# Kernel tuning notes

Measured on AMD Instinct MI355X. Metric: run time of the kernel, lower is better.

## Reference

```python
import jax, jax.numpy as jnp
import numpy as np

N_NODES = 100000
N_EDGES = 800000
N_ETYPES = 5
IN_DIM = 23
HID_DIM = 128
OUT_DIM = 64
NUM_GRAPHS = 64


def setup_inputs() -> dict:
    key = jax.random.key(0)
    ks = jax.random.split(key, 8)
    feat = jax.random.normal(ks[0], (N_NODES, IN_DIM), dtype=jnp.float32)
    src = jax.random.randint(ks[1], (N_ETYPES, N_EDGES), 0, N_NODES, dtype=jnp.int32)
    dst = jax.random.randint(ks[2], (N_ETYPES, N_EDGES), 0, N_NODES, dtype=jnp.int32)
    graph_ids = jnp.sort(jax.random.randint(ks[3], (N_NODES,), 0, NUM_GRAPHS, dtype=jnp.int32))
    W1 = jax.random.normal(ks[4], (N_ETYPES, IN_DIM, HID_DIM), dtype=jnp.float32) * 0.1
    b1 = jnp.zeros((N_ETYPES, HID_DIM), dtype=jnp.float32)
    W2 = jax.random.normal(ks[5], (N_ETYPES, HID_DIM, OUT_DIM), dtype=jnp.float32) * 0.1
    b2 = jnp.zeros((N_ETYPES, OUT_DIM), dtype=jnp.float32)
    return {"feat": feat, "src": src, "dst": dst, "graph_ids": graph_ids,
            "W1": W1, "b1": b1, "W2": W2, "b2": b2}


def _hetero_sage_layer(h, src, dst, W, b):
    """HeteroGraphConv of SAGEConv(aggregator='gcn') summed over edge types.
    gcn aggregator: h_neigh[i] = (sum_{j->i} h[j] + h[i]) / (in_deg(i) + 1);
    per-etype output = h_neigh @ W_e + b_e; combine with sum."""
    n = h.shape[0]
    out = jnp.zeros((n, W.shape[-1]), dtype=h.dtype)
    ones_e = jnp.ones((src.shape[1],), dtype=h.dtype)
    for e in range(N_ETYPES):
        deg = jax.ops.segment_sum(ones_e, dst[e], num_segments=n)          # [N]
        agg = jax.ops.segment_sum(h[src[e]], dst[e], num_segments=n)       # [N, D]
        h_neigh = (agg + h) / (deg + 1.0)[:, None]
        out = out + h_neigh @ W[e] + b[e]
    return out


def reference(feat, src, dst, graph_ids, W1, b1, W2, b2):
    # layer 1: in_dim -> hid, relu (dropout in eval mode = identity)
    h = jax.nn.relu(_hetero_sage_layer(feat, src, dst, W1, b1))
    # layer 2: hid -> out (no activation)
    h = _hetero_sage_layer(h, src, dst, W2, b2)
    # dgl.mean_nodes: per-graph mean over nodes
    counts = jax.ops.segment_sum(jnp.ones((h.shape[0],), h.dtype), graph_ids,
                                 num_segments=NUM_GRAPHS)
    sums = jax.ops.segment_sum(h, graph_ids, num_segments=NUM_GRAPHS)
    return sums / jnp.maximum(counts, 1.0)[:, None]
```

## Files before the change

### kernel.cpp

```cpp
#include <hip/hip_runtime.h>

#define N_NODES   100000
#define N_EDGES   800000
#define N_ETYPES  5
#define IN_DIM    23
#define FPAD      32
#define HID_DIM   128
#define OUT_DIM   64
#define NUM_GRAPHS 64
#define NBKT      391
#define PBLK      125
#define CHUNK     6400
#define PN        (N_ETYPES*NBKT*PBLK)
#define SCAN_NBLK ((PN + 1023) / 1024)
#define TOT_EDGES (N_ETYPES*N_EDGES)
#define BKT_CAP   3072
#define ASTR      136
#define A1STR     40


__device__ __forceinline__ unsigned short f2bf(float x) {
    unsigned u = __float_as_uint(x);
    unsigned r = (u + 0x7FFFu + ((u >> 16) & 1u)) >> 16;
    return (unsigned short)r;
}
__device__ __forceinline__ float bf2f(unsigned short h) {
    return __uint_as_float(((unsigned)h) << 16);
}

typedef __attribute__((ext_vector_type(8))) short bf16x8;
typedef __attribute__((ext_vector_type(4))) float f32x4;
typedef __attribute__((ext_vector_type(2))) float f32x2;

__global__ __launch_bounds__(256) void cvt_feat_k(const float* __restrict__ feat,
                                                  unsigned short* __restrict__ fb32) {
    int i = blockIdx.x * 256 + threadIdx.x;
    if (i < N_NODES * FPAD) {
        int n = i >> 5, d = i & 31;
        fb32[i] = (d < IN_DIM) ? f2bf(feat[n * IN_DIM + d]) : (unsigned short)0;
    }
}

__global__ __launch_bounds__(256) void cvt_w2t_k(const float* __restrict__ W2,
                                                 unsigned short* __restrict__ w2tb) {
    int i = blockIdx.x * 256 + threadIdx.x;
    if (i < N_ETYPES * OUT_DIM * HID_DIM) {
        int e = i / (OUT_DIM * HID_DIM);
        int r = i - e * (OUT_DIM * HID_DIM);
        int n = r >> 7, k = r & 127;
        w2tb[i] = f2bf(W2[(e * HID_DIM + k) * OUT_DIM + n]);
    }
}

__global__ __launch_bounds__(256) void cvt_w1t_k(const float* __restrict__ W1,
                                                 unsigned short* __restrict__ w1tb) {
    int i = blockIdx.x * 256 + threadIdx.x;
    if (i < N_ETYPES * HID_DIM * 32) {
        int e = i / (HID_DIM * 32);
        int r = i - e * (HID_DIM * 32);
        int n = r >> 5, k = r & 31;
        w1tb[i] = (k < IN_DIM) ? f2bf(W1[e * IN_DIM * HID_DIM + k * HID_DIM + n])
                               : (unsigned short)0;
    }
}

__global__ __launch_bounds__(128) void cvt_b1s_k(const float* __restrict__ b1,
                                                 float* __restrict__ b1s) {
    int d = threadIdx.x;
    float s = 0.f;
    for (int e = 0; e < N_ETYPES; e++) s += b1[e * HID_DIM + d];
    b1s[d] = s;
}

__global__ __launch_bounds__(256) void part1_k(const int* __restrict__ dst,
                                               int* __restrict__ hp) {
    __shared__ int hist[NBKT];
    int e = blockIdx.y, blk = blockIdx.x, t = threadIdx.x;
    for (int b = t; b < NBKT; b += 256) hist[b] = 0;
    __syncthreads();
    const int* dp = dst + e * N_EDGES + blk * CHUNK;
    for (int k = t; k < CHUNK; k += 256) atomicAdd(&hist[dp[k] >> 8], 1);
    __syncthreads();
    for (int b = t; b < NBKT; b += 256) hp[(e * NBKT + b) * PBLK + blk] = hist[b];
}

__global__ __launch_bounds__(256) void scan1_k(const int* __restrict__ in,
                                               int* __restrict__ out,
                                               int* __restrict__ bsum) {
    __shared__ int ls[256];
    int t = threadIdx.x;
    int base = blockIdx.x * 1024 + t * 4;
    int v[4]; int s = 0;
    for (int j = 0; j < 4; j++) { int i = base + j; v[j] = (i < PN) ? in[i] : 0; s += v[j]; }
    ls[t] = s; __syncthreads();
    for (int o = 1; o < 256; o <<= 1) {
        int x = (t >= o) ? ls[t - o] : 0;
        __syncthreads();
        ls[t] += x;
        __syncthreads();
    }
    int run = (t > 0) ? ls[t - 1] : 0;
    if (t == 255) bsum[blockIdx.x] = ls[255];
    for (int j = 0; j < 4; j++) { int i = base + j; if (i < PN) out[i] = run; run += v[j]; }
}

__global__ __launch_bounds__(256) void scan2_k(int* __restrict__ bsum) {
    __shared__ int ls[256];
    int t = threadIdx.x;
    int v = (t < SCAN_NBLK) ? bsum[t] : 0;
    ls[t] = v; __syncthreads();
    for (int o = 1; o < 256; o <<= 1) {
        int x = (t >= o) ? ls[t - o] : 0;
        __syncthreads();
        ls[t] += x;
        __syncthreads();
    }
    if (t < SCAN_NBLK) bsum[t] = (t > 0) ? ls[t - 1] : 0;
}

__global__ __launch_bounds__(256) void scan3_k(int* __restrict__ off,
                                               const int* __restrict__ bsum) {
    int i = blockIdx.x * 256 + threadIdx.x;
    if (i < PN) off[i] += bsum[i >> 10];
}

__global__ __launch_bounds__(256) void part2_k(const int* __restrict__ src,
                                               const int* __restrict__ dst,
                                               const int* __restrict__ off,
                                               unsigned* __restrict__ ep) {
    __shared__ int cur[NBKT];
    int e = blockIdx.y, blk = blockIdx.x, t = threadIdx.x;
    for (int b = t; b < NBKT; b += 256) cur[b] = off[(e * NBKT + b) * PBLK + blk];
    __syncthreads();
    const int* dp = dst + e * N_EDGES + blk * CHUNK;
    const int* sp = src + e * N_EDGES + blk * CHUNK;
    for (int k = t; k < CHUNK; k += 256) {
        int d = dp[k], s = sp[k];
        int b = d >> 8;
        int pos = atomicAdd(&cur[b], 1);
        ep[pos] = (unsigned)s | ((unsigned)(d & 255) << 24);
    }
}

__global__ __launch_bounds__(256) void sort_k(const int* __restrict__ off,
                                              const unsigned* __restrict__ ep,
                                              unsigned* __restrict__ csr,
                                              int* __restrict__ noff,
                                              int* __restrict__ degn,
                                              float* __restrict__ inv) {
    __shared__ unsigned recs[BKT_CAP];
    __shared__ int hist[256];
    __shared__ int scn[256];
    __shared__ int curp[256];
    int b = blockIdx.x, e = blockIdx.y, t = threadIdx.x;
    int lin = (e * NBKT + b) * PBLK;
    int S = off[lin];
    int E = (lin == PN - PBLK) ? TOT_EDGES : off[lin + PBLK];
    int cnt = E - S;
    hist[t] = 0;
    __syncthreads();
    for (int i = t; i < cnt; i += 256) {
        unsigned r = ep[S + i];
        recs[i] = r;
        atomicAdd(&hist[r >> 24], 1);
    }
    __syncthreads();
    scn[t] = hist[t];
    __syncthreads();
    for (int o = 1; o < 256; o <<= 1) {
        int x = (t >= o) ? scn[t - o] : 0;
        __syncthreads();
        scn[t] += x;
        __syncthreads();
    }
    int excl = scn[t] - hist[t];
    curp[t] = excl;
    int n = b * 256 + t;
    if (n < N_NODES) {
        noff[e * N_NODES + n] = S + excl;
        degn[e * N_NODES + n] = hist[t];
        inv[e * N_NODES + n]  = 1.f / (float)(hist[t] + 1);
    }
    __syncthreads();
    for (int i = t; i < cnt; i += 256) {
        unsigned r = recs[i];
        int pos = atomicAdd(&curp[r >> 24], 1);
        csr[S + pos] = r & 0xFFFFFFu;
    }
}

__global__ __launch_bounds__(256) void agg1_k(const int* __restrict__ noff,
                                              const int* __restrict__ degn,
                                              const unsigned* __restrict__ csr,
                                              const unsigned short* __restrict__ fb32,
                                              const float* __restrict__ inv,
                                              unsigned short* __restrict__ agg1b) {
    int e = blockIdx.y;
    int t = threadIdx.x;
    int lane = t & 15;
    int n = blockIdx.x * 16 + (t >> 4);
    int idx = e * N_NODES + n;
    int st = noff[idx];
    int cnt = degn[idx];
    ushort2 sv = *(const ushort2*)&fb32[n * FPAD + lane * 2];
    float a0 = bf2f(sv.x), a1 = bf2f(sv.y);
    int k = 0;
    for (; k + 3 < cnt; k += 4) {
        int s0 = csr[st + k];
        int s1 = csr[st + k + 1];
        int s2 = csr[st + k + 2];
        int s3 = csr[st + k + 3];
        ushort2 v0 = *(const ushort2*)&fb32[s0 * FPAD + lane * 2];
        ushort2 v1 = *(const ushort2*)&fb32[s1 * FPAD + lane * 2];
        ushort2 v2 = *(const ushort2*)&fb32[s2 * FPAD + lane * 2];
        ushort2 v3 = *(const ushort2*)&fb32[s3 * FPAD + lane * 2];
        a0 += bf2f(v0.x) + bf2f(v1.x) + bf2f(v2.x) + bf2f(v3.x);
        a1 += bf2f(v0.y) + bf2f(v1.y) + bf2f(v2.y) + bf2f(v3.y);
    }
    for (; k < cnt; k++) {
        int s0 = csr[st + k];
        ushort2 v0 = *(const ushort2*)&fb32[s0 * FPAD + lane * 2];
        a0 += bf2f(v0.x);
        a1 += bf2f(v0.y);
    }
    float iv = inv[idx];
    ushort2 o; o.x = f2bf(a0 * iv); o.y = f2bf(a1 * iv);
    *(ushort2*)&agg1b[(size_t)idx * 32 + lane * 2] = o;
}

__global__ __launch_bounds__(256) void gemm1_k(const unsigned short* __restrict__ agg1b,
                                               const unsigned short* __restrict__ w1tb,
                                               const float* __restrict__ b1s,
                                               unsigned short* __restrict__ h1b) {
    __shared__ unsigned short As[64 * A1STR];
    __shared__ unsigned short Wt[128 * A1STR];
    int t = threadIdx.x;
    int node0 = blockIdx.x * 64;
    int w = t >> 6, lane = t & 63;
    int m = lane & 15, quad = lane >> 4;

    f32x4 acc[8];
    for (int nt = 0; nt < 8; nt++) {
        float bb = b1s[nt * 16 + m];
        f32x4 c = {bb, bb, bb, bb};
        acc[nt] = c;
    }

    for (int e = 0; e < N_ETYPES; e++) {
        __syncthreads();
        for (int j = t; j < 64 * 8; j += 256) {
            int n = j >> 3, c4 = (j & 7) * 4;
            int gn = node0 + n;
            int cn = gn < N_NODES ? gn : N_NODES - 1;
            *(ushort4*)&As[n * A1STR + c4] =
                *(const ushort4*)&agg1b[(size_t)(e * N_NODES + cn) * 32 + c4];
        }
        for (int j = t; j < 128 * 8; j += 256) {
            int n = j >> 3, c4 = (j & 7) * 4;
            *(ushort4*)&Wt[n * A1STR + c4] =
                *(const ushort4*)&w1tb[(size_t)(e * HID_DIM + n) * 32 + c4];
        }
        __syncthreads();
        bf16x8 a = *(const bf16x8*)&As[(w * 16 + m) * A1STR + quad * 8];
        for (int nt = 0; nt < 8; nt++) {
            bf16x8 b = *(const bf16x8*)&Wt[(nt * 16 + m) * A1STR + quad * 8];
            acc[nt] = __builtin_amdgcn_mfma_f32_16x16x32_bf16(a, b, acc[nt], 0, 0, 0);
        }
    }
    for (int nt = 0; nt < 8; nt++) {
        for (int r = 0; r < 4; r++) {
            int gn = node0 + w * 16 + quad * 4 + r;
            if (gn < N_NODES)
                h1b[(size_t)gn * HID_DIM + nt * 16 + m] = f2bf(fmaxf(acc[nt][r], 0.f));
        }
    }
}

__global__ __launch_bounds__(256) void gemm2_k(const unsigned short* __restrict__ h1b,
                                               const unsigned short* __restrict__ w2tb,
                                               unsigned char* __restrict__ t2f8) {
    __shared__ unsigned short As[64 * ASTR];
    __shared__ unsigned short Wt[64 * ASTR];
    int t = threadIdx.x;
    int node0 = blockIdx.x * 64;
    int w = t >> 6, lane = t & 63;
    int m = lane & 15, quad = lane >> 4;

    for (int j = t; j < 64 * 32; j += 256) {
        int n = j >> 5, c4 = (j & 31) * 4;
        int gn = node0 + n;
        int cn = gn < N_NODES ? gn : N_NODES - 1;
        *(ushort4*)&As[n * ASTR + c4] = *(const ushort4*)&h1b[cn * HID_DIM + c4];
    }
    __syncthreads();
    bf16x8 a[4];
    for (int ks = 0; ks < 4; ks++)
        a[ks] = *(const bf16x8*)&As[(w * 16 + m) * ASTR + ks * 32 + quad * 8];

    for (int e = 0; e < N_ETYPES; e++) {
        __syncthreads();
        for (int j = t; j < 64 * 32; j += 256) {
            int n = j >> 5, c4 = (j & 31) * 4;
            *(ushort4*)&Wt[n * ASTR + c4] =
                *(const ushort4*)&w2tb[(e * OUT_DIM + n) * HID_DIM + c4];
        }
        __syncthreads();
        unsigned char* out = t2f8 + (size_t)e * N_NODES * OUT_DIM;
        for (int nt = 0; nt < 4; nt++) {
            f32x4 c = {0.f, 0.f, 0.f, 0.f};
            for (int ks = 0; ks < 4; ks++) {
                bf16x8 b = *(const bf16x8*)&Wt[(nt * 16 + m) * ASTR + ks * 32 + quad * 8];
                c = __builtin_amdgcn_mfma_f32_16x16x32_bf16(a[ks], b, c, 0, 0, 0);
            }
            for (int r = 0; r < 4; r++) {
                int gn = node0 + w * 16 + quad * 4 + r;
                if (gn < N_NODES) {
                    int p = __builtin_amdgcn_cvt_pk_fp8_f32(c[r], c[r], 0, false);
                    out[(size_t)gn * OUT_DIM + nt * 16 + m] = (unsigned char)(p & 0xFF);
                }
            }
        }
    }
}

__global__ __launch_bounds__(256) void gather2_k(const int* __restrict__ noff,
                                                 const int* __restrict__ degn,
                                                 const float* __restrict__ inv,
                                                 const unsigned* __restrict__ csr,
                                                 const unsigned char* __restrict__ t2f8,
                                                 const int* __restrict__ gid,
                                                 float* __restrict__ gsum) {
    __shared__ float4 red4[16 * 4 * 16];
    int b = blockIdx.x, qb = blockIdx.y, t = threadIdx.x;
    int lane = t & 15, ng = t >> 4;
    int nbase = b * 256 + qb * 32;
    int gbase = nbase < N_NODES ? nbase : N_NODES - 1;
    int g0 = gid[gbase];
    float4 f[2];
    f[0] = make_float4(0.f, 0.f, 0.f, 0.f);
    f[1] = make_float4(0.f, 0.f, 0.f, 0.f);

    for (int e = 0; e < N_ETYPES; e++) {
        const unsigned char* base = t2f8 + (size_t)e * N_NODES * OUT_DIM;
        #pragma unroll
        for (int pass = 0; pass < 2; pass++) {
            int n = nbase + pass * 16 + ng;
            if (n >= N_NODES) break;
            int idx = e * N_NODES + n;
            int st = noff[idx];
            int cnt = degn[idx];
            float iv = inv[idx];
            unsigned rv = *(const unsigned*)&base[(size_t)n * OUT_DIM + lane * 4];
            f32x2 lo = __builtin_amdgcn_cvt_pk_f32_fp8((int)rv, false);
            f32x2 hi = __builtin_amdgcn_cvt_pk_f32_fp8((int)rv, true);
            float ax = lo.x, ay = lo.y, az = hi.x, aw = hi.y;
            int k = 0;
            for (; k + 3 < cnt; k += 4) {
                int sA = csr[st + k];
                int sB = csr[st + k + 1];
                int sC = csr[st + k + 2];
                int sD = csr[st + k + 3];
                unsigned rA = *(const unsigned*)&base[(size_t)sA * OUT_DIM + lane * 4];
                unsigned rB = *(const unsigned*)&base[(size_t)sB * OUT_DIM + lane * 4];
                unsigned rC = *(const unsigned*)&base[(size_t)sC * OUT_DIM + lane * 4];
                unsigned rD = *(const unsigned*)&base[(size_t)sD * OUT_DIM + lane * 4];
                f32x2 lA = __builtin_amdgcn_cvt_pk_f32_fp8((int)rA, false);
                f32x2 hA = __builtin_amdgcn_cvt_pk_f32_fp8((int)rA, true);
                f32x2 lB = __builtin_amdgcn_cvt_pk_f32_fp8((int)rB, false);
                f32x2 hB = __builtin_amdgcn_cvt_pk_f32_fp8((int)rB, true);
                f32x2 lC = __builtin_amdgcn_cvt_pk_f32_fp8((int)rC, false);
                f32x2 hC = __builtin_amdgcn_cvt_pk_f32_fp8((int)rC, true);
                f32x2 lD = __builtin_amdgcn_cvt_pk_f32_fp8((int)rD, false);
                f32x2 hD = __builtin_amdgcn_cvt_pk_f32_fp8((int)rD, true);
                ax += (lA.x + lB.x) + (lC.x + lD.x);
                ay += (lA.y + lB.y) + (lC.y + lD.y);
                az += (hA.x + hB.x) + (hC.x + hD.x);
                aw += (hA.y + hB.y) + (hC.y + hD.y);
            }
            for (; k < cnt; k++) {
                int sA = csr[st + k];
                unsigned rA = *(const unsigned*)&base[(size_t)sA * OUT_DIM + lane * 4];
                f32x2 lA = __builtin_amdgcn_cvt_pk_f32_fp8((int)rA, false);
                f32x2 hA = __builtin_amdgcn_cvt_pk_f32_fp8((int)rA, true);
                ax += lA.x; ay += lA.y; az += hA.x; aw += hA.y;
            }
            f[pass].x += iv * ax; f[pass].y += iv * ay;
            f[pass].z += iv * az; f[pass].w += iv * aw;
        }
    }

    float4 sa0 = {0,0,0,0}, sa1 = {0,0,0,0}, sa2 = {0,0,0,0}, sa3 = {0,0,0,0};
    #pragma unroll
    for (int pass = 0; pass < 2; pass++) {
        int n = nbase + pass * 16 + ng;
        if (n >= N_NODES) break;
        float4 v = f[pass];
        int slot = gid[n] - g0;
        float m0 = (slot == 0) ? 1.f : 0.f;
        float m1 = (slot == 1) ? 1.f : 0.f;
        float m2 = (slot == 2) ? 1.f : 0.f;
        float m3 = (slot == 3) ? 1.f : 0.f;
        sa0.x += m0 * v.x; sa0.y += m0 * v.y; sa0.z += m0 * v.z; sa0.w += m0 * v.w;
        sa1.x += m1 * v.x; sa1.y += m1 * v.y; sa1.z += m1 * v.z; sa1.w += m1 * v.w;
        sa2.x += m2 * v.x; sa2.y += m2 * v.y; sa2.z += m2 * v.z; sa2.w += m2 * v.w;
        sa3.x += m3 * v.x; sa3.y += m3 * v.y; sa3.z += m3 * v.z; sa3.w += m3 * v.w;
        if (slot > 3) {
            atomicAdd(&gsum[(g0 + slot) * 64 + lane * 4 + 0], v.x);
            atomicAdd(&gsum[(g0 + slot) * 64 + lane * 4 + 1], v.y);
            atomicAdd(&gsum[(g0 + slot) * 64 + lane * 4 + 2], v.z);
            atomicAdd(&gsum[(g0 + slot) * 64 + lane * 4 + 3], v.w);
        }
    }
    red4[(ng * 4 + 0) * 16 + lane] = sa0;
    red4[(ng * 4 + 1) * 16 + lane] = sa1;
    red4[(ng * 4 + 2) * 16 + lane] = sa2;
    red4[(ng * 4 + 3) * 16 + lane] = sa3;
    __syncthreads();
    const float* red = (const float*)red4;
    int slot = t >> 6, d = t & 63;
    float s = 0.f;
    for (int j = 0; j < 16; j++) s += red[(j * 4 + slot) * 64 + d];
    int g = g0 + slot;
    if (g < NUM_GRAPHS) atomicAdd(&gsum[g * 64 + d], s);
}

__global__ __launch_bounds__(256) void gcnt_k(const int* __restrict__ gid,
                                              float* __restrict__ gcnt) {
    __shared__ int h[NUM_GRAPHS];
    int b = blockIdx.x, t = threadIdx.x;
    if (t < NUM_GRAPHS) h[t] = 0;
    __syncthreads();
    int n = b * 256 + t;
    if (n < N_NODES) atomicAdd(&h[gid[n]], 1);
    __syncthreads();
    if (t < NUM_GRAPHS && h[t] > 0) atomicAdd(&gcnt[t], (float)h[t]);
}

__global__ __launch_bounds__(256) void final_k(const float* __restrict__ gsum,
                                               const float* __restrict__ gcnt,
                                               const float* __restrict__ b2,
                                               float* __restrict__ out) {
    int idx = blockIdx.x * 256 + threadIdx.x;
    if (idx >= NUM_GRAPHS * OUT_DIM) return;
    int d = idx & 63;
    float B2 = 0.f;
    for (int e = 0; e < N_ETYPES; e++) B2 += b2[e * OUT_DIM + d];
    float c = gcnt[idx >> 6];
    out[idx] = (gsum[idx] + c * B2) / fmaxf(c, 1.0f);
}

extern "C" void kernel_launch(void* const* d_in, const int* in_sizes, int n_in,
                              void* d_out, int out_size, void* d_ws, size_t ws_size,
                              hipStream_t stream) {
    const float* feat = (const float*)d_in[0];
    const int*   src  = (const int*)d_in[1];
    const int*   dst  = (const int*)d_in[2];
    const int*   gid  = (const int*)d_in[3];
    const float* W1   = (const float*)d_in[4];
    const float* b1   = (const float*)d_in[5];
    const float* W2   = (const float*)d_in[6];
    const float* b2   = (const float*)d_in[7];

    float* ws = (float*)d_ws;
    int*            HP   = (int*)ws;
    int*            OFFP = (int*)ws + 245000;
    int*            BSUM = (int*)ws + 490000;
    float*          INV  = ws + 490512;
    int*            NOFF = (int*)ws + 990512;
    int*            DEGN = (int*)ws + 1490512;
    unsigned short* FB32 = (unsigned short*)(ws + 1990512);
    float*          GSUM = ws + 3590512;
    float*          GCNT = ws + 3594608;
    unsigned*       EP   = (unsigned*)(ws + 3595000);
    unsigned short* AGG1B= (unsigned short*)(ws + 7595000);
    unsigned char*  T2F8 = (unsigned char*)(ws + 3595000);
    unsigned short* H1B  = (unsigned short*)(ws + 15595000);
    unsigned*       CSR  = (unsigned*)(ws + 21995000);
    unsigned short* W2TB = (unsigned short*)(ws + 25995000);
    unsigned short* W1TB = (unsigned short*)(ws + 26015480);
    float*          B1S  = ws + 26025720;

    hipMemsetAsync(GSUM, 0, (size_t)(4096 + 64) * sizeof(float), stream);

    cvt_feat_k<<<(N_NODES * FPAD + 255) / 256, 256, 0, stream>>>(feat, FB32);
    cvt_w2t_k<<<(N_ETYPES * OUT_DIM * HID_DIM + 255) / 256, 256, 0, stream>>>(W2, W2TB);
    cvt_w1t_k<<<(N_ETYPES * HID_DIM * 32 + 255) / 256, 256, 0, stream>>>(W1, W1TB);
    cvt_b1s_k<<<1, 128, 0, stream>>>(b1, B1S);
    part1_k<<<dim3(PBLK, N_ETYPES), 256, 0, stream>>>(dst, HP);
    scan1_k<<<SCAN_NBLK, 256, 0, stream>>>(HP, OFFP, BSUM);
    scan2_k<<<1, 256, 0, stream>>>(BSUM);
    scan3_k<<<(PN + 255) / 256, 256, 0, stream>>>(OFFP, BSUM);
    part2_k<<<dim3(PBLK, N_ETYPES), 256, 0, stream>>>(src, dst, OFFP, EP);
    sort_k<<<dim3(NBKT, N_ETYPES), 256, 0, stream>>>(OFFP, EP, CSR, NOFF, DEGN, INV);

    agg1_k<<<dim3(6250, N_ETYPES), 256, 0, stream>>>(NOFF, DEGN, CSR, FB32, INV, AGG1B);
    gemm1_k<<<(N_NODES + 63) / 64, 256, 0, stream>>>(AGG1B, W1TB, B1S, H1B);
    gemm2_k<<<(N_NODES + 63) / 64, 256, 0, stream>>>(H1B, W2TB, T2F8);
    gather2_k<<<dim3(NBKT, 8), 256, 0, stream>>>(NOFF, DEGN, INV, CSR, T2F8, gid, GSUM);

    gcnt_k<<<391, 256, 0, stream>>>(gid, GCNT);
    final_k<<<16, 256, 0, stream>>>(GSUM, GCNT, b2, (float*)d_out);
}
```

Baseline: 424.8 us.

## Fuse layer GEMMs via shared-memory H1, merge weight conversions, widen gather2 lanes

```diff
diff --git a/kernel.cpp b/kernel.cpp
--- a/kernel.cpp
+++ b/kernel.cpp
@@ -41,8 +41,12 @@
     }
 }
 
-__global__ __launch_bounds__(256) void cvt_w2t_k(const float* __restrict__ W2,
-                                                 unsigned short* __restrict__ w2tb) {
+__global__ __launch_bounds__(256) void cvt_w_k(const float* __restrict__ W1,
+                                               const float* __restrict__ b1,
+                                               const float* __restrict__ W2,
+                                               unsigned short* __restrict__ w1tb,
+                                               unsigned short* __restrict__ w2tb,
+                                               float* __restrict__ b1s) {
     int i = blockIdx.x * 256 + threadIdx.x;
     if (i < N_ETYPES * OUT_DIM * HID_DIM) {
         int e = i / (OUT_DIM * HID_DIM);
@@ -50,11 +54,6 @@
         int n = r >> 7, k = r & 127;
         w2tb[i] = f2bf(W2[(e * HID_DIM + k) * OUT_DIM + n]);
     }
-}
-
-__global__ __launch_bounds__(256) void cvt_w1t_k(const float* __restrict__ W1,
-                                                 unsigned short* __restrict__ w1tb) {
-    int i = blockIdx.x * 256 + threadIdx.x;
     if (i < N_ETYPES * HID_DIM * 32) {
         int e = i / (HID_DIM * 32);
         int r = i - e * (HID_DIM * 32);
@@ -62,14 +61,11 @@
         w1tb[i] = (k < IN_DIM) ? f2bf(W1[e * IN_DIM * HID_DIM + k * HID_DIM + n])
                                : (unsigned short)0;
     }
-}
-
-__global__ __launch_bounds__(128) void cvt_b1s_k(const float* __restrict__ b1,
-                                                 float* __restrict__ b1s) {
-    int d = threadIdx.x;
-    float s = 0.f;
-    for (int e = 0; e < N_ETYPES; e++) s += b1[e * HID_DIM + d];
-    b1s[d] = s;
+    if (i < HID_DIM) {
+        float s = 0.f;
+        for (int e = 0; e < N_ETYPES; e++) s += b1[e * HID_DIM + i];
+        b1s[i] = s;
+    }
 }
 
 __global__ __launch_bounds__(256) void part1_k(const int* __restrict__ dst,
@@ -228,12 +224,15 @@
     *(ushort2*)&agg1b[(size_t)idx * 32 + lane * 2] = o;
 }
 
-__global__ __launch_bounds__(256) void gemm1_k(const unsigned short* __restrict__ agg1b,
-                                               const unsigned short* __restrict__ w1tb,
-                                               const float* __restrict__ b1s,
-                                               unsigned short* __restrict__ h1b) {
-    __shared__ unsigned short As[64 * A1STR];
-    __shared__ unsigned short Wt[128 * A1STR];
+__global__ __launch_bounds__(256) void gemm12_k(const unsigned short* __restrict__ agg1b,
+                                                const unsigned short* __restrict__ w1tb,
+                                                const float* __restrict__ b1s,
+                                                const unsigned short* __restrict__ w2tb,
+                                                unsigned char* __restrict__ t2f8) {
+    __shared__ unsigned short H1s[64 * ASTR];
+    __shared__ unsigned short Wt2[64 * ASTR];
+    unsigned short* As1 = Wt2;
+    unsigned short* Wt1 = Wt2 + 64 * A1STR;
     int t = threadIdx.x;
     int node0 = blockIdx.x * 64;
     int w = t >> 6, lane = t & 63;
@@ -245,63 +244,42 @@
         f32x4 c = {bb, bb, bb, bb};
         acc[nt] = c;
     }
-
     for (int e = 0; e < N_ETYPES; e++) {
         __syncthreads();
         for (int j = t; j < 64 * 8; j += 256) {
             int n = j >> 3, c4 = (j & 7) * 4;
             int gn = node0 + n;
             int cn = gn < N_NODES ? gn : N_NODES - 1;
-            *(ushort4*)&As[n * A1STR + c4] =
+            *(ushort4*)&As1[n * A1STR + c4] =
                 *(const ushort4*)&agg1b[(size_t)(e * N_NODES + cn) * 32 + c4];
         }
         for (int j = t; j < 128 * 8; j += 256) {
             int n = j >> 3, c4 = (j & 7) * 4;
-            *(ushort4*)&Wt[n * A1STR + c4] =
+            *(ushort4*)&Wt1[n * A1STR + c4] =
                 *(const ushort4*)&w1tb[(size_t)(e * HID_DIM + n) * 32 + c4];
         }
         __syncthreads();
-        bf16x8 a = *(const bf16x8*)&As[(w * 16 + m) * A1STR + quad * 8];
+        bf16x8 a = *(const bf16x8*)&As1[(w * 16 + m) * A1STR + quad * 8];
         for (int nt = 0; nt < 8; nt++) {
-            bf16x8 b = *(const bf16x8*)&Wt[(nt * 16 + m) * A1STR + quad * 8];
+            bf16x8 b = *(const bf16x8*)&Wt1[(nt * 16 + m) * A1STR + quad * 8];
             acc[nt] = __builtin_amdgcn_mfma_f32_16x16x32_bf16(a, b, acc[nt], 0, 0, 0);
         }
     }
-    for (int nt = 0; nt < 8; nt++) {
-        for (int r = 0; r < 4; r++) {
-            int gn = node0 + w * 16 + quad * 4 + r;
-            if (gn < N_NODES)
-                h1b[(size_t)gn * HID_DIM + nt * 16 + m] = f2bf(fmaxf(acc[nt][r], 0.f));
-        }
-    }
-}
-
-__global__ __launch_bounds__(256) void gemm2_k(const unsigned short* __restrict__ h1b,
-                                               const unsigned short* __restrict__ w2tb,
-                                               unsigned char* __restrict__ t2f8) {
-    __shared__ unsigned short As[64 * ASTR];
-    __shared__ unsigned short Wt[64 * ASTR];
-    int t = threadIdx.x;
-    int node0 = blockIdx.x * 64;
-    int w = t >> 6, lane = t & 63;
-    int m = lane & 15, quad = lane >> 4;
-
-    for (int j = t; j < 64 * 32; j += 256) {
-        int n = j >> 5, c4 = (j & 31) * 4;
-        int gn = node0 + n;
-        int cn = gn < N_NODES ? gn : N_NODES - 1;
-        *(ushort4*)&As[n * ASTR + c4] = *(const ushort4*)&h1b[cn * HID_DIM + c4];
-    }
-    __syncthreads();
-    bf16x8 a[4];
+    __syncthreads();
+    for (int nt = 0; nt < 8; nt++)
+        for (int r = 0; r < 4; r++)
+            H1s[(w * 16 + quad * 4 + r) * ASTR + nt * 16 + m] =
+                f2bf(fmaxf(acc[nt][r], 0.f));
+    __syncthreads();
+
+    bf16x8 a2[4];
     for (int ks = 0; ks < 4; ks++)
-        a[ks] = *(const bf16x8*)&As[(w * 16 + m) * ASTR + ks * 32 + quad * 8];
-
+        a2[ks] = *(const bf16x8*)&H1s[(w * 16 + m) * ASTR + ks * 32 + quad * 8];
     for (int e = 0; e < N_ETYPES; e++) {
         __syncthreads();
         for (int j = t; j < 64 * 32; j += 256) {
             int n = j >> 5, c4 = (j & 31) * 4;
-            *(ushort4*)&Wt[n * ASTR + c4] =
+            *(ushort4*)&Wt2[n * ASTR + c4] =
                 *(const ushort4*)&w2tb[(e * OUT_DIM + n) * HID_DIM + c4];
         }
         __syncthreads();
@@ -309,8 +287,8 @@
         for (int nt = 0; nt < 4; nt++) {
             f32x4 c = {0.f, 0.f, 0.f, 0.f};
             for (int ks = 0; ks < 4; ks++) {
-                bf16x8 b = *(const bf16x8*)&Wt[(nt * 16 + m) * ASTR + ks * 32 + quad * 8];
-                c = __builtin_amdgcn_mfma_f32_16x16x32_bf16(a[ks], b, c, 0, 0, 0);
+                bf16x8 b = *(const bf16x8*)&Wt2[(nt * 16 + m) * ASTR + ks * 32 + quad * 8];
+                c = __builtin_amdgcn_mfma_f32_16x16x32_bf16(a2[ks], b, c, 0, 0, 0);
             }
             for (int r = 0; r < 4; r++) {
                 int gn = node0 + w * 16 + quad * 4 + r;
@@ -330,97 +308,91 @@
                                                  const unsigned char* __restrict__ t2f8,
                                                  const int* __restrict__ gid,
                                                  float* __restrict__ gsum) {
-    __shared__ float4 red4[16 * 4 * 16];
+    __shared__ float red[32 * 64];
+    __shared__ int slotl[32];
     int b = blockIdx.x, qb = blockIdx.y, t = threadIdx.x;
-    int lane = t & 15, ng = t >> 4;
+    int lane = t & 7, ng = t >> 3;
     int nbase = b * 256 + qb * 32;
     int gbase = nbase < N_NODES ? nbase : N_NODES - 1;
     int g0 = gid[gbase];
-    float4 f[2];
-    f[0] = make_float4(0.f, 0.f, 0.f, 0.f);
-    f[1] = make_float4(0.f, 0.f, 0.f, 0.f);
-
-    for (int e = 0; e < N_ETYPES; e++) {
-        const unsigned char* base = t2f8 + (size_t)e * N_NODES * OUT_DIM;
-        #pragma unroll
-        for (int pass = 0; pass < 2; pass++) {
-            int n = nbase + pass * 16 + ng;
-            if (n >= N_NODES) break;
+    if (t < 32) {
+        int nn = nbase + t;
+        slotl[t] = (nn < N_NODES) ? gid[nn] - g0 : -1;
+    }
+    __syncthreads();
+    int n = nbase + ng;
+    float f0=0,f1=0,f2=0,f3=0,f4=0,f5=0,f6=0,f7=0;
+    if (n < N_NODES) {
+        for (int e = 0; e < N_ETYPES; e++) {
+            const unsigned char* base = t2f8 + (size_t)e * N_NODES * OUT_DIM;
             int idx = e * N_NODES + n;
             int st = noff[idx];
             int cnt = degn[idx];
             float iv = inv[idx];
-            unsigned rv = *(const unsigned*)&base[(size_t)n * OUT_DIM + lane * 4];
-            f32x2 lo = __builtin_amdgcn_cvt_pk_f32_fp8((int)rv, false);
-            f32x2 hi = __builtin_amdgcn_cvt_pk_f32_fp8((int)rv, true);
-            float ax = lo.x, ay = lo.y, az = hi.x, aw = hi.y;
+            uint2 rv = *(const uint2*)&base[(size_t)n * OUT_DIM + lane * 8];
+            f32x2 l0 = __builtin_amdgcn_cvt_pk_f32_fp8((int)rv.x, false);
+            f32x2 h0 = __builtin_amdgcn_cvt_pk_f32_fp8((int)rv.x, true);
+            f32x2 l1 = __builtin_amdgcn_cvt_pk_f32_fp8((int)rv.y, false);
+            f32x2 h1 = __builtin_amdgcn_cvt_pk_f32_fp8((int)rv.y, true);
+            float a0=l0.x,a1=l0.y,a2=h0.x,a3=h0.y,a4=l1.x,a5=l1.y,a6=h1.x,a7=h1.y;
             int k = 0;
             for (; k + 3 < cnt; k += 4) {
                 int sA = csr[st + k];
                 int sB = csr[st + k + 1];
                 int sC = csr[st + k + 2];
                 int sD = csr[st + k + 3];
-                unsigned rA = *(const unsigned*)&base[(size_t)sA * OUT_DIM + lane * 4];
-                unsigned rB = *(const unsigned*)&base[(size_t)sB * OUT_DIM + lane * 4];
-                unsigned rC = *(const unsigned*)&base[(size_t)sC * OUT_DIM + lane * 4];
-                unsigned rD = *(const unsigned*)&base[(size_t)sD * OUT_DIM + lane * 4];
-                f32x2 lA = __builtin_amdgcn_cvt_pk_f32_fp8((int)rA, false);
-                f32x2 hA = __builtin_amdgcn_cvt_pk_f32_fp8((int)rA, true);
-                f32x2 lB = __builtin_amdgcn_cvt_pk_f32_fp8((int)rB, false);
-                f32x2 hB = __builtin_amdgcn_cvt_pk_f32_fp8((int)rB, true);
-                f32x2 lC = __builtin_amdgcn_cvt_pk_f32_fp8((int)rC, false);
-                f32x2 hC = __builtin_amdgcn_cvt_pk_f32_fp8((int)rC, true);
-                f32x2 lD = __builtin_amdgcn_cvt_pk_f32_fp8((int)rD, false);
-                f32x2 hD = __builtin_amdgcn_cvt_pk_f32_fp8((int)rD, true);
-                ax += (lA.x + lB.x) + (lC.x + lD.x);
-                ay += (lA.y + lB.y) + (lC.y + lD.y);
-                az += (hA.x + hB.x) + (hC.x + hD.x);
-                aw += (hA.y + hB.y) + (hC.y + hD.y);
+                uint2 rA = *(const uint2*)&base[(size_t)sA * OUT_DIM + lane * 8];
+                uint2 rB = *(const uint2*)&base[(size_t)sB * OUT_DIM + lane * 8];
+                uint2 rC = *(const uint2*)&base[(size_t)sC * OUT_DIM + lane * 8];
+                uint2 rD = *(const uint2*)&base[(size_t)sD * OUT_DIM + lane * 8];
+                f32x2 v;
+                v = __builtin_amdgcn_cvt_pk_f32_fp8((int)rA.x, false); a0+=v.x; a1+=v.y;
+                v = __builtin_amdgcn_cvt_pk_f32_fp8((int)rA.x, true);  a2+=v.x; a3+=v.y;
+                v = __builtin_amdgcn_cvt_pk_f32_fp8((int)rA.y, false); a4+=v.x; a5+=v.y;
+                v = __builtin_amdgcn_cvt_pk_f32_fp8((int)rA.y, true);  a6+=v.x; a7+=v.y;
+                v = __builtin_amdgcn_cvt_pk_f32_fp8((int)rB.x, false); a0+=v.x; a1+=v.y;
+                v = __builtin_amdgcn_cvt_pk_f32_fp8((int)rB.x, true);  a2+=v.x; a3+=v.y;
+                v = __builtin_amdgcn_cvt_pk_f32_fp8((int)rB.y, false); a4+=v.x; a5+=v.y;
+                v = __builtin_amdgcn_cvt_pk_f32_fp8((int)rB.y, true);  a6+=v.x; a7+=v.y;
+                v = __builtin_amdgcn_cvt_pk_f32_fp8((int)rC.x, false); a0+=v.x; a1+=v.y;
+                v = __builtin_amdgcn_cvt_pk_f32_fp8((int)rC.x, true);  a2+=v.x; a3+=v.y;
+                v = __builtin_amdgcn_cvt_pk_f32_fp8((int)rC.y, false); a4+=v.x; a5+=v.y;
+                v = __builtin_amdgcn_cvt_pk_f32_fp8((int)rC.y, true);  a6+=v.x; a7+=v.y;
+                v = __builtin_amdgcn_cvt_pk_f32_fp8((int)rD.x, false); a0+=v.x; a1+=v.y;
+                v = __builtin_amdgcn_cvt_pk_f32_fp8((int)rD.x, true);  a2+=v.x; a3+=v.y;
+                v = __builtin_amdgcn_cvt_pk_f32_fp8((int)rD.y, false); a4+=v.x; a5+=v.y;
+                v = __builtin_amdgcn_cvt_pk_f32_fp8((int)rD.y, true);  a6+=v.x; a7+=v.y;
             }
             for (; k < cnt; k++) {
                 int sA = csr[st + k];
-                unsigned rA = *(const unsigned*)&base[(size_t)sA * OUT_DIM + lane * 4];
-                f32x2 lA = __builtin_amdgcn_cvt_pk_f32_fp8((int)rA, false);
-                f32x2 hA = __builtin_amdgcn_cvt_pk_f32_fp8((int)rA, true);
-                ax += lA.x; ay += lA.y; az += hA.x; aw += hA.y;
+                uint2 rA = *(const uint2*)&base[(size_t)sA * OUT_DIM + lane * 8];
+                f32x2 v;
+                v = __builtin_amdgcn_cvt_pk_f32_fp8((int)rA.x, false); a0+=v.x; a1+=v.y;
+                v = __builtin_amdgcn_cvt_pk_f32_fp8((int)rA.x, true);  a2+=v.x; a3+=v.y;
+                v = __builtin_amdgcn_cvt_pk_f32_fp8((int)rA.y, false); a4+=v.x; a5+=v.y;
+                v = __builtin_amdgcn_cvt_pk_f32_fp8((int)rA.y, true);  a6+=v.x; a7+=v.y;
             }
-            f[pass].x += iv * ax; f[pass].y += iv * ay;
-            f[pass].z += iv * az; f[pass].w += iv * aw;
-        }
-    }
-
-    float4 sa0 = {0,0,0,0}, sa1 = {0,0,0,0}, sa2 = {0,0,0,0}, sa3 = {0,0,0,0};
-    #pragma unroll
-    for (int pass = 0; pass < 2; pass++) {
-        int n = nbase + pass * 16 + ng;
-        if (n >= N_NODES) break;
-        float4 v = f[pass];
-        int slot = gid[n] - g0;
-        float m0 = (slot == 0) ? 1.f : 0.f;
-        float m1 = (slot == 1) ? 1.f : 0.f;
-        float m2 = (slot == 2) ? 1.f : 0.f;
-        float m3 = (slot == 3) ? 1.f : 0.f;
-        sa0.x += m0 * v.x; sa0.y += m0 * v.y; sa0.z += m0 * v.z; sa0.w += m0 * v.w;
-        sa1.x += m1 * v.x; sa1.y += m1 * v.y; sa1.z += m1 * v.z; sa1.w += m1 * v.w;
-        sa2.x += m2 * v.x; sa2.y += m2 * v.y; sa2.z += m2 * v.z; sa2.w += m2 * v.w;
-        sa3.x += m3 * v.x; sa3.y += m3 * v.y; sa3.z += m3 * v.z; sa3.w += m3 * v.w;
-        if (slot > 3) {
-            atomicAdd(&gsum[(g0 + slot) * 64 + lane * 4 + 0], v.x);
-            atomicAdd(&gsum[(g0 + slot) * 64 + lane * 4 + 1], v.y);
-            atomicAdd(&gsum[(g0 + slot) * 64 + lane * 4 + 2], v.z);
-            atomicAdd(&gsum[(g0 + slot) * 64 + lane * 4 + 3], v.w);
-        }
-    }
-    red4[(ng * 4 + 0) * 16 + lane] = sa0;
-    red4[(ng * 4 + 1) * 16 + lane] = sa1;
-    red4[(ng * 4 + 2) * 16 + lane] = sa2;
-    red4[(ng * 4 + 3) * 16 + lane] = sa3;
-    __syncthreads();
-    const float* red = (const float*)red4;
-    int slot = t >> 6, d = t & 63;
+            f0+=iv*a0; f1+=iv*a1; f2+=iv*a2; f3+=iv*a3;
+            f4+=iv*a4; f5+=iv*a5; f6+=iv*a6; f7+=iv*a7;
+        }
+    }
+    int slot = slotl[ng];
+    if (slot > 3 && n < N_NODES) {
+        int gbase8 = (g0 + slot) * 64 + lane * 8;
+        atomicAdd(&gsum[gbase8 + 0], f0); atomicAdd(&gsum[gbase8 + 1], f1);
+        atomicAdd(&gsum[gbase8 + 2], f2); atomicAdd(&gsum[gbase8 + 3], f3);
+        atomicAdd(&gsum[gbase8 + 4], f4); atomicAdd(&gsum[gbase8 + 5], f5);
+        atomicAdd(&gsum[gbase8 + 6], f6); atomicAdd(&gsum[gbase8 + 7], f7);
+        f0=f1=f2=f3=f4=f5=f6=f7=0.f;
+    }
+    *(float4*)&red[ng * 64 + lane * 8]     = make_float4(f0, f1, f2, f3);
+    *(float4*)&red[ng * 64 + lane * 8 + 4] = make_float4(f4, f5, f6, f7);
+    __syncthreads();
+    int slot2 = t >> 6, d = t & 63;
     float s = 0.f;
-    for (int j = 0; j < 16; j++) s += red[(j * 4 + slot) * 64 + d];
-    int g = g0 + slot;
+    for (int j = 0; j < 32; j++)
+        s += (slotl[j] == slot2) ? red[j * 64 + d] : 0.f;
+    int g = g0 + slot2;
     if (g < NUM_GRAPHS) atomicAdd(&gsum[g * 64 + d], s);
 }
 
@@ -474,18 +446,17 @@
     unsigned*       EP   = (unsigned*)(ws + 3595000);
     unsigned short* AGG1B= (unsigned short*)(ws + 7595000);
     unsigned char*  T2F8 = (unsigned char*)(ws + 3595000);
-    unsigned short* H1B  = (unsigned short*)(ws + 15595000);
-    unsigned*       CSR  = (unsigned*)(ws + 21995000);
-    unsigned short* W2TB = (unsigned short*)(ws + 25995000);
-    unsigned short* W1TB = (unsigned short*)(ws + 26015480);
-    float*          B1S  = ws + 26025720;
+    T2F8 = (unsigned char*)(ws + 15595000);
+    unsigned*       CSR  = (unsigned*)(ws + 23595000);
+    unsigned short* W2TB = (unsigned short*)(ws + 27595000);
+    unsigned short* W1TB = (unsigned short*)(ws + 27615480);
+    float*          B1S  = ws + 27625720;
 
     hipMemsetAsync(GSUM, 0, (size_t)(4096 + 64) * sizeof(float), stream);
 
     cvt_feat_k<<<(N_NODES * FPAD + 255) / 256, 256, 0, stream>>>(feat, FB32);
-    cvt_w2t_k<<<(N_ETYPES * OUT_DIM * HID_DIM + 255) / 256, 256, 0, stream>>>(W2, W2TB);
-    cvt_w1t_k<<<(N_ETYPES * HID_DIM * 32 + 255) / 256, 256, 0, stream>>>(W1, W1TB);
-    cvt_b1s_k<<<1, 128, 0, stream>>>(b1, B1S);
+    cvt_w_k<<<(N_ETYPES * OUT_DIM * HID_DIM + 255) / 256, 256, 0, stream>>>(
+        W1, b1, W2, W1TB, W2TB, B1S);
     part1_k<<<dim3(PBLK, N_ETYPES), 256, 0, stream>>>(dst, HP);
     scan1_k<<<SCAN_NBLK, 256, 0, stream>>>(HP, OFFP, BSUM);
     scan2_k<<<1, 256, 0, stream>>>(BSUM);
@@ -494,8 +465,7 @@
     sort_k<<<dim3(NBKT, N_ETYPES), 256, 0, stream>>>(OFFP, EP, CSR, NOFF, DEGN, INV);
 
     agg1_k<<<dim3(6250, N_ETYPES), 256, 0, stream>>>(NOFF, DEGN, CSR, FB32, INV, AGG1B);
-    gemm1_k<<<(N_NODES + 63) / 64, 256, 0, stream>>>(AGG1B, W1TB, B1S, H1B);
-    gemm2_k<<<(N_NODES + 63) / 64, 256, 0, stream>>>(H1B, W2TB, T2F8);
+    gemm12_k<<<(N_NODES + 63) / 64, 256, 0, stream>>>(AGG1B, W1TB, B1S, W2TB, T2F8);
     gather2_k<<<dim3(NBKT, 8), 256, 0, stream>>>(NOFF, DEGN, INV, CSR, T2F8, gid, GSUM);
 
     gcnt_k<<<391, 256, 0, stream>>>(gid, GCNT);
```

New measurement: 416.7 us. No clear change (-1.9%).
